# Performance work log

Measured on AMD Instinct MI355X. Metric: run time of the kernel, lower is better.

The kernel has to match this reference:

```python
import jax, jax.numpy as jnp
import numpy as np

B, S, D, H = 4, 2048, 512, 8

def setup_inputs() -> dict:
    key = jax.random.key(0)
    ks = jax.random.split(key, 6)
    query = jax.random.normal(ks[0], (B, S, D), dtype=jnp.float32)
    value = jax.random.normal(ks[1], (B, S, D), dtype=jnp.float32)
    # causal additive mask, broadcast over heads: [H, S, S]
    causal = jnp.where(jnp.tril(jnp.ones((S, S), dtype=bool)), 0.0, -1e9).astype(jnp.float32)
    mask = jnp.broadcast_to(causal[None, :, :], (H, S, S))
    sd = 1.0 / np.sqrt(D)
    Wq = jax.random.normal(ks[2], (D, D), dtype=jnp.float32) * sd
    Wkv = jax.random.normal(ks[3], (D, 2 * D), dtype=jnp.float32) * sd
    Wo = jax.random.normal(ks[4], (D, D), dtype=jnp.float32) * sd
    normalizer = jnp.asarray(1.0 / np.sqrt(D // H), dtype=jnp.float32)  # 1/sqrt(head_size)
    head_mults = jnp.ones((1, 1, H, 1), dtype=jnp.float32)
    return {"query": query, "value": value, "mask": mask, "Wq": Wq, "Wkv": Wkv,
            "Wo": Wo, "normalizer": normalizer, "head_mults": head_mults}

def reference(query, value, mask, Wq, Wkv, Wo, normalizer, head_mults):
    b, sq, d = query.shape
    h = head_mults.shape[2]
    q = (query @ Wq).reshape(b, sq, h, -1)                 # [b,q,h,hd]
    k, v = jnp.split(value @ Wkv, 2, axis=-1)
    sk = value.shape[1]
    k = k.reshape(b, sk, h, -1)
    v = v.reshape(b, sk, h, -1)
    score = jnp.einsum('bqhd,bkhd->bhqk', q, k) * normalizer
    score = score + mask[None, :, :, :]
    align = jax.nn.softmax(score, axis=-1)
    heads = jnp.einsum('bhqk,bkhd->bqhd', align, v)        # [b,q,h,hd]
    # cross-head normalization (over head axis, ddof=0 like tf.reduce_std)
    mean = jnp.mean(heads, axis=-2, keepdims=True)
    std = jnp.std(heads, axis=-2, keepdims=True)
    heads = (heads - mean) / (std + 0.01)
    heads = heads * head_mults
    out = heads.reshape(b, sq, d) @ Wo
    return out
```

## Files before the change

### kernel.cpp

```cpp
#include <hip/hip_runtime.h>


typedef float  f32x4  __attribute__((ext_vector_type(4)));
typedef __bf16 bf16x8 __attribute__((ext_vector_type(8)));
typedef short  s16x4  __attribute__((ext_vector_type(4)));
typedef unsigned short u16;

#define BS 2048
#define DD 512
#define NH 8

__device__ __forceinline__ u16 f2bf(float f) {
  union { float f; unsigned u; } v; v.f = f;
  unsigned r = v.u + 0x7fffu + ((v.u >> 16) & 1u);
  return (u16)(r >> 16);
}
__device__ __forceinline__ float bf2f(u16 b) {
  union { unsigned u; float f; } v; v.u = ((unsigned)b) << 16; return v.f;
}
__device__ __forceinline__ u16 cvt1(float f) {
  __bf16 h = (__bf16)f;
  return __builtin_bit_cast(u16, h);
}

__device__ __forceinline__ void gll16(const u16* g, u16* l) {
  __builtin_amdgcn_global_load_lds((const __attribute__((address_space(1))) void*)g,
                                   (__attribute__((address_space(3))) void*)l, 16, 0, 0);
}

__global__ __launch_bounds__(256) void prep(const float* __restrict__ query,
                                            const float* __restrict__ value,
                                            const float* __restrict__ Wq,
                                            const float* __restrict__ Wkv,
                                            const float* __restrict__ Wo,
                                            u16* __restrict__ Qf, u16* __restrict__ Vf,
                                            u16* __restrict__ WqT, u16* __restrict__ WkvT,
                                            u16* __restrict__ WoT) {
  __shared__ float Ts[64][65];
  const int t = threadIdx.x;
  int tb = blockIdx.x;
  if (tb < 2048) {
    const float* s = (tb < 1024) ? query : value;
    u16* d = (tb < 1024) ? Qf : Vf;
    long off = (long)(tb & 1023) * 4096 + (long)t * 16;
    const float* sp = s + off;
    float4 x0 = *(const float4*)sp;
    float4 x1 = *(const float4*)(sp + 4);
    float4 x2 = *(const float4*)(sp + 8);
    float4 x3 = *(const float4*)(sp + 12);
    bf16x8 o0, o1;
    o0[0] = (__bf16)x0.x; o0[1] = (__bf16)x0.y; o0[2] = (__bf16)x0.z; o0[3] = (__bf16)x0.w;
    o0[4] = (__bf16)x1.x; o0[5] = (__bf16)x1.y; o0[6] = (__bf16)x1.z; o0[7] = (__bf16)x1.w;
    o1[0] = (__bf16)x2.x; o1[1] = (__bf16)x2.y; o1[2] = (__bf16)x2.z; o1[3] = (__bf16)x2.w;
    o1[4] = (__bf16)x3.x; o1[5] = (__bf16)x3.y; o1[6] = (__bf16)x3.z; o1[7] = (__bf16)x3.w;
    u16* dp = d + off;
    *(bf16x8*)dp = o0;
    *(bf16x8*)(dp + 8) = o1;
    return;
  }
  tb -= 2048;
  const float* W; u16* Wt; int N, ntn;
  if (tb < 64)       { W = Wq;  Wt = WqT;  N = 512;  ntn = 8; }
  else if (tb < 192) { W = Wkv; Wt = WkvT; N = 1024; ntn = 16; tb -= 64; }
  else               { W = Wo;  Wt = WoT;  N = 512;  ntn = 8;  tb -= 192; }
  int tk = tb / ntn, tn = tb - tk * ntn;
  int r = t >> 2, c0 = (t & 3) * 16;
  const float* src = &W[(long)(tk * 64 + r) * N + tn * 64 + c0];
#pragma unroll
  for (int j = 0; j < 4; ++j) {
    float4 x = *(const float4*)(src + j * 4);
    Ts[r][c0 + j * 4 + 0] = x.x; Ts[r][c0 + j * 4 + 1] = x.y;
    Ts[r][c0 + j * 4 + 2] = x.z; Ts[r][c0 + j * 4 + 3] = x.w;
  }
  __syncthreads();
  u16* dst = &Wt[(long)(tn * 64 + r) * 512 + tk * 64 + c0];
#pragma unroll
  for (int m = 0; m < 4; ++m) {
    ushort4 o;
    o.x = f2bf(Ts[c0 + m * 4 + 0][r]); o.y = f2bf(Ts[c0 + m * 4 + 1][r]);
    o.z = f2bf(Ts[c0 + m * 4 + 2][r]); o.w = f2bf(Ts[c0 + m * 4 + 3][r]);
    *(ushort4*)(dst + m * 4) = o;
  }
}

__device__ __forceinline__ void gemm_core64(const u16* __restrict__ A,
                                            const u16* __restrict__ Bt,
                                            int m0, int n0, int K,
                                            u16* Al, u16* Bl, f32x4 acc[4][4]) {
  const int t = threadIdx.x;
  const int wv = t >> 6, ln = t & 63, qd = ln >> 4, l16 = ln & 15;
  const int rw = (wv & 1) * 64, cw = (wv >> 1) * 64;
  const int srB = wv * 16 + (ln >> 2), scB = (ln & 3) * 8;
  for (int k0 = 0; k0 < K; k0 += 64) {
    __syncthreads();
#pragma unroll
    for (int p = 0; p < 2; ++p)
#pragma unroll
      for (int c = 0; c < 2; ++c) {
        int r = c * 64 + srB;
        gll16(&A[(long)(m0 + r) * K + k0 + p * 32 + scB], &Al[p * 4096 + r * 32 + scB]);
      }
#pragma unroll
    for (int p = 0; p < 2; ++p)
#pragma unroll
      for (int c = 0; c < 2; ++c) {
        int r = c * 64 + srB;
        gll16(&Bt[(long)(n0 + r) * K + k0 + p * 32 + scB], &Bl[p * 4096 + r * 32 + scB]);
      }
    __syncthreads();
#pragma unroll
    for (int p = 0; p < 2; ++p) {
      bf16x8 af[4], bfr[4];
#pragma unroll
      for (int i = 0; i < 4; ++i)
        af[i] = *(const bf16x8*)&Al[p * 4096 + (rw + i * 16 + l16) * 32 + qd * 8];
#pragma unroll
      for (int j = 0; j < 4; ++j)
        bfr[j] = *(const bf16x8*)&Bl[p * 4096 + (cw + j * 16 + l16) * 32 + qd * 8];
#pragma unroll
      for (int i = 0; i < 4; ++i)
#pragma unroll
        for (int j = 0; j < 4; ++j)
          acc[i][j] = __builtin_amdgcn_mfma_f32_16x16x32_bf16(af[i], bfr[j], acc[i][j], 0, 0, 0);
    }
  }
}

__global__ __launch_bounds__(256) void qkv_gemm(const u16* __restrict__ Qf,
                                                const u16* __restrict__ Vf,
                                                const u16* __restrict__ WqT,
                                                const u16* __restrict__ WkvT,
                                                u16* __restrict__ Qb,
                                                u16* __restrict__ Kb,
                                                u16* __restrict__ Vt) {
  __shared__ __align__(16) u16 Al[2 * 128 * 32];
  __shared__ __align__(16) u16 Bl[2 * 128 * 32];
  const bool isQ = blockIdx.y < 4;
  const u16* A = isQ ? Qf : Vf;
  const u16* Bt = isQ ? WqT : WkvT;
  const int n0 = (isQ ? blockIdx.y : blockIdx.y - 4) * 128;
  const int m0 = blockIdx.x * 128;
  f32x4 acc[4][4] = {};
  gemm_core64(A, Bt, m0, n0, 512, Al, Bl, acc);
  const int t = threadIdx.x;
  const int wv = t >> 6, ln = t & 63, qd = ln >> 4, l16 = ln & 15;
  const int rw = (wv & 1) * 64, cw = (wv >> 1) * 64;
  if (isQ) {
#pragma unroll
    for (int i = 0; i < 4; ++i)
#pragma unroll
      for (int j = 0; j < 4; ++j) {
        int row = m0 + rw + i * 16 + qd * 4, col = n0 + cw + j * 16 + l16;
#pragma unroll
        for (int r = 0; r < 4; ++r)
          Qb[(long)(row + r) * 512 + col] = cvt1(acc[i][j][r]);
      }
  } else {
#pragma unroll
    for (int j = 0; j < 4; ++j) {
      int col = n0 + cw + j * 16 + l16;
      if (col < 512) {
#pragma unroll
        for (int i = 0; i < 4; ++i) {
          int row = m0 + rw + i * 16 + qd * 4;
#pragma unroll
          for (int r = 0; r < 4; ++r)
            Kb[(long)(row + r) * 512 + col] = cvt1(acc[i][j][r]);
        }
      } else {
        int c2 = col - 512, hh = c2 >> 6, dd = c2 & 63;
#pragma unroll
        for (int i = 0; i < 4; ++i) {
          int sg = m0 + rw + i * 16 + qd * 4;
          int bb = sg >> 11, ss = sg & 2047;
          ushort4 o;
          o.x = cvt1(acc[i][j][0]); o.y = cvt1(acc[i][j][1]);
          o.z = cvt1(acc[i][j][2]); o.w = cvt1(acc[i][j][3]);
          *(ushort4*)&Vt[((long)(bb * 8 + hh) * 64 + dd) * 2048 + ss] = o;
        }
      }
    }
  }
}

__global__ __launch_bounds__(256) void out_gemm(const u16* __restrict__ A,
                                                const u16* __restrict__ Bt,
                                                float* __restrict__ C) {
  __shared__ __align__(16) u16 Al[2 * 128 * 32];
  __shared__ __align__(16) u16 Bl[2 * 128 * 32];
  const int m0 = blockIdx.x * 128, n0 = blockIdx.y * 128;
  f32x4 acc[4][4] = {};
  gemm_core64(A, Bt, m0, n0, 512, Al, Bl, acc);
  const int t = threadIdx.x;
  const int wv = t >> 6, ln = t & 63, qd = ln >> 4, l16 = ln & 15;
  const int rw = (wv & 1) * 64, cw = (wv >> 1) * 64;
#pragma unroll
  for (int i = 0; i < 4; ++i)
#pragma unroll
    for (int j = 0; j < 4; ++j) {
      int row = m0 + rw + i * 16 + qd * 4, col = n0 + cw + j * 16 + l16;
#pragma unroll
      for (int r = 0; r < 4; ++r)
        C[(long)(row + r) * 512 + col] = acc[i][j][r];
    }
}

__device__ __forceinline__ void attn_phase(const u16* ks, const u16* vs,
                                           const bf16x8 bq[2], f32x4 o[4],
                                           float& l_i, float scale2, bool diag,
                                           int wv, int qd, int l16) {
  constexpr int ST = 72;
  f32x4 s[4] = {};
#pragma unroll
  for (int c = 0; c < 2; ++c)
#pragma unroll
    for (int nt = 0; nt < 4; ++nt) {
      bf16x8 ak = *(const bf16x8*)&ks[(nt * 16 + l16) * ST + c * 32 + qd * 8];
      s[nt] = __builtin_amdgcn_mfma_f32_16x16x32_bf16(ak, bq[c], s[nt], 0, 0, 0);
    }
  if (diag) {
    const int limi = wv * 16 + l16;
#pragma unroll
    for (int nt = 0; nt < 4; ++nt)
#pragma unroll
      for (int r = 0; r < 4; ++r) {
        float v = s[nt][r] * scale2;
        if (nt * 16 + qd * 4 + r > limi) v = -INFINITY;
        float p = exp2f(v);
        s[nt][r] = p;
        l_i += p;
      }
  } else {
#pragma unroll
    for (int nt = 0; nt < 4; ++nt)
#pragma unroll
      for (int r = 0; r < 4; ++r) {
        float p = exp2f(s[nt][r] * scale2);
        s[nt][r] = p;
        l_i += p;
      }
  }
#pragma unroll
  for (int cp = 0; cp < 2; ++cp) {
    bf16x8 pb;
#pragma unroll
    for (int j = 0; j < 4; ++j) {
      pb[j] = (__bf16)s[cp * 2][j];
      pb[4 + j] = (__bf16)s[cp * 2 + 1][j];
    }
#pragma unroll
    for (int n2 = 0; n2 < 4; ++n2) {
      bf16x8 av;
      s16x4* ah = (s16x4*)&av;
      const u16* vp = &vs[(n2 * 16 + l16) * ST + cp * 32 + qd * 4];
      ah[0] = *(const s16x4*)vp;
      ah[1] = *(const s16x4*)(vp + 16);
      o[n2] = __builtin_amdgcn_mfma_f32_16x16x32_bf16(av, pb, o[n2], 0, 0, 0);
    }
  }
}

__global__ __launch_bounds__(256, 2) void attn(const u16* __restrict__ Qb,
                                               const u16* __restrict__ Kb,
                                               const u16* __restrict__ Vt,
                                               u16* __restrict__ heads,
                                               const float* __restrict__ normp) {
  constexpr int ST = 72;
  __shared__ __align__(16) u16 Ks[2][64 * ST];
  __shared__ __align__(16) u16 Vts[2][64 * ST];
  const float scale2 = normp[0] * 1.44269504f;
  const int t = threadIdx.x;
  const int wv = t >> 6, ln = t & 63, qd = ln >> 4, l16 = ln & 15;
  const int sr = t >> 2, scg = (t & 3) * 16;
  const int h = blockIdx.y, b = blockIdx.z;
  const int bs0 = b * BS;
  const u16* vtb = Vt + ((long)(b * 8 + h) * 64) * 2048;
  const int qtS = blockIdx.x, qtL = 31 - qtS;

  bf16x8 bqS[2], bqL[2];
#pragma unroll
  for (int c = 0; c < 2; ++c) {
    bqS[c] = *(const bf16x8*)&Qb[(long)(bs0 + qtS * 64 + wv * 16 + l16) * 512 + h * 64 + c * 32 + qd * 8];
    bqL[c] = *(const bf16x8*)&Qb[(long)(bs0 + qtL * 64 + wv * 16 + l16) * 512 + h * 64 + c * 32 + qd * 8];
  }

  bf16x8 kr0, kr1, vr0, vr1;
#define FETCH(KB) do { \
    const u16* kp_ = &Kb[(long)(bs0 + (KB) * 64 + sr) * 512 + h * 64 + scg]; \
    kr0 = *(const bf16x8*)kp_; kr1 = *(const bf16x8*)(kp_ + 8); \
    const u16* vp_ = &vtb[(long)sr * 2048 + (KB) * 64 + scg]; \
    vr0 = *(const bf16x8*)vp_; vr1 = *(const bf16x8*)(vp_ + 8); } while (0)
  FETCH(0);
  float lS = 0.f, lL = 0.f;
  f32x4 oS[4] = {}, oL[4] = {};

  for (int kb = 0; kb <= qtL; ++kb) {
    const int buf = kb & 1;
    *(bf16x8*)&Ks[buf][sr * ST + scg] = kr0;
    *(bf16x8*)&Ks[buf][sr * ST + scg + 8] = kr1;
    *(bf16x8*)&Vts[buf][sr * ST + scg] = vr0;
    *(bf16x8*)&Vts[buf][sr * ST + scg + 8] = vr1;
    __syncthreads();
    if (kb < qtL) FETCH(kb + 1);

    attn_phase(Ks[buf], Vts[buf], bqL, oL, lL, scale2, kb == qtL, wv, qd, l16);
    if (kb <= qtS)
      attn_phase(Ks[buf], Vts[buf], bqS, oS, lS, scale2, kb == qtS, wv, qd, l16);
  }
#undef FETCH

  lL += __shfl_xor(lL, 16); lL += __shfl_xor(lL, 32);
  lS += __shfl_xor(lS, 16); lS += __shfl_xor(lS, 32);
  float invL = 1.f / lL, invS = 1.f / lS;
  __syncthreads();
#pragma unroll
  for (int n2 = 0; n2 < 4; ++n2)
#pragma unroll
    for (int r = 0; r < 4; ++r) {
      Ks[0][(wv * 16 + l16) * ST + n2 * 16 + qd * 4 + r] = cvt1(oL[n2][r] * invL);
      Vts[0][(wv * 16 + l16) * ST + n2 * 16 + qd * 4 + r] = cvt1(oS[n2][r] * invS);
    }
  __syncthreads();
  {
    u16* dstL = &heads[(long)(bs0 + qtL * 64 + sr) * 512 + h * 64 + scg];
    *(bf16x8*)dstL = *(const bf16x8*)&Ks[0][sr * ST + scg];
    *(bf16x8*)(dstL + 8) = *(const bf16x8*)&Ks[0][sr * ST + scg + 8];
    u16* dstS = &heads[(long)(bs0 + qtS * 64 + sr) * 512 + h * 64 + scg];
    *(bf16x8*)dstS = *(const bf16x8*)&Vts[0][sr * ST + scg];
    *(bf16x8*)(dstS + 8) = *(const bf16x8*)&Vts[0][sr * ST + scg + 8];
  }
}

__global__ __launch_bounds__(256) void headnorm(const u16* __restrict__ heads,
                                                const float* __restrict__ hm,
                                                u16* __restrict__ outn) {
  int i = blockIdx.x * 256 + threadIdx.x;
  int d8 = (i & 7) * 8;
  long bs = i >> 3;
  const u16* p = heads + bs * DD + d8;
  float x[NH][8];
  float mean[8] = {0.f, 0.f, 0.f, 0.f, 0.f, 0.f, 0.f, 0.f};
#pragma unroll
  for (int h = 0; h < NH; ++h) {
    bf16x8 v = *(const bf16x8*)(p + h * 64);
#pragma unroll
    for (int j = 0; j < 8; ++j) { x[h][j] = (float)v[j]; mean[j] += x[h][j]; }
  }
#pragma unroll
  for (int j = 0; j < 8; ++j) mean[j] *= 0.125f;
  float var[8] = {0.f, 0.f, 0.f, 0.f, 0.f, 0.f, 0.f, 0.f};
#pragma unroll
  for (int h = 0; h < NH; ++h)
#pragma unroll
    for (int j = 0; j < 8; ++j) { float dd = x[h][j] - mean[j]; var[j] += dd * dd; }
  float inv[8];
#pragma unroll
  for (int j = 0; j < 8; ++j) inv[j] = 1.f / (sqrtf(var[j] * 0.125f) + 0.01f);
  u16* q = outn + bs * DD + d8;
#pragma unroll
  for (int h = 0; h < NH; ++h) {
    float m = hm[h];
    bf16x8 o;
#pragma unroll
    for (int j = 0; j < 8; ++j) o[j] = (__bf16)((x[h][j] - mean[j]) * inv[j] * m);
    *(bf16x8*)(q + h * 64) = o;
  }
}

extern "C" void kernel_launch(void* const* d_in, const int* in_sizes, int n_in,
                              void* d_out, int out_size, void* d_ws, size_t ws_size,
                              hipStream_t stream) {
  const float* query = (const float*)d_in[0];
  const float* value = (const float*)d_in[1];
  const float* Wq    = (const float*)d_in[3];
  const float* Wkv   = (const float*)d_in[4];
  const float* Wo    = (const float*)d_in[5];
  const float* normp = (const float*)d_in[6];
  const float* hmult = (const float*)d_in[7];

  char* ws = (char*)d_ws;
  const size_t MB = 1 << 20;
  u16*   WqT   = (u16*)(ws);
  u16*   WkvT  = (u16*)(ws + 524288);
  u16*   WoT   = (u16*)(ws + 1 * MB + 524288);
  u16*   Qb    = (u16*)(ws + 2 * MB);
  u16*   Kb    = (u16*)(ws + 10 * MB);
  u16*   Vt    = (u16*)(ws + 18 * MB);
  u16*   heads = (u16*)(ws + 26 * MB);
  u16*   hN    = (u16*)(ws + 34 * MB);
  u16*   Qf    = (u16*)(ws + 42 * MB);
  u16*   Vf    = (u16*)(ws + 50 * MB);

  prep<<<2304, 256, 0, stream>>>(query, value, Wq, Wkv, Wo, Qf, Vf, WqT, WkvT, WoT);
  qkv_gemm<<<dim3(64, 12), 256, 0, stream>>>(Qf, Vf, WqT, WkvT, Qb, Kb, Vt);
  attn<<<dim3(16, NH, 4), 256, 0, stream>>>(Qb, Kb, Vt, heads, normp);
  headnorm<<<(4 * BS * 64) / 512, 256, 0, stream>>>(heads, hmult, hN);
  out_gemm<<<dim3(64, 4), 256, 0, stream>>>(hN, WoT, (float*)d_out);
}
```

Measured before the change: 286.2 us.

## Split paired causal query tiles into one tile per block, raise occupancy

Each attention block used to process a short and a long query tile together to balance causal work, sharing K/V loads between them. Now each block handles a single 64-row query tile, the grid doubles to 32 tiles, and launch bounds request 4 blocks per CU. This gives more parallelism and lower register pressure, at the cost of losing K/V reuse across the paired tiles and leaving per-block work unbalanced, so the long tiles may dominate the tail.

Measured after the change: 307.4 us. +7.4%, slower.

```diff
diff --git a/kernel.cpp b/kernel.cpp
--- a/kernel.cpp
+++ b/kernel.cpp
@@ -260,7 +260,7 @@
   }
 }
 
-__global__ __launch_bounds__(256, 2) void attn(const u16* __restrict__ Qb,
+__global__ __launch_bounds__(256, 4) void attn(const u16* __restrict__ Qb,
                                                const u16* __restrict__ Kb,
                                                const u16* __restrict__ Vt,
                                                u16* __restrict__ heads,
@@ -275,14 +275,12 @@
   const int h = blockIdx.y, b = blockIdx.z;
   const int bs0 = b * BS;
   const u16* vtb = Vt + ((long)(b * 8 + h) * 64) * 2048;
-  const int qtS = blockIdx.x, qtL = 31 - qtS;
-
-  bf16x8 bqS[2], bqL[2];
-#pragma unroll
-  for (int c = 0; c < 2; ++c) {
-    bqS[c] = *(const bf16x8*)&Qb[(long)(bs0 + qtS * 64 + wv * 16 + l16) * 512 + h * 64 + c * 32 + qd * 8];
-    bqL[c] = *(const bf16x8*)&Qb[(long)(bs0 + qtL * 64 + wv * 16 + l16) * 512 + h * 64 + c * 32 + qd * 8];
-  }
+  const int qt = blockIdx.x;
+
+  bf16x8 bq[2];
+#pragma unroll
+  for (int c = 0; c < 2; ++c)
+    bq[c] = *(const bf16x8*)&Qb[(long)(bs0 + qt * 64 + wv * 16 + l16) * 512 + h * 64 + c * 32 + qd * 8];
 
   bf16x8 kr0, kr1, vr0, vr1;
 #define FETCH(KB) do { \
@@ -291,43 +289,35 @@
     const u16* vp_ = &vtb[(long)sr * 2048 + (KB) * 64 + scg]; \
     vr0 = *(const bf16x8*)vp_; vr1 = *(const bf16x8*)(vp_ + 8); } while (0)
   FETCH(0);
-  float lS = 0.f, lL = 0.f;
-  f32x4 oS[4] = {}, oL[4] = {};
-
-  for (int kb = 0; kb <= qtL; ++kb) {
+  float l_i = 0.f;
+  f32x4 o[4] = {};
+
+  for (int kb = 0; kb <= qt; ++kb) {
     const int buf = kb & 1;
     *(bf16x8*)&Ks[buf][sr * ST + scg] = kr0;
     *(bf16x8*)&Ks[buf][sr * ST + scg + 8] = kr1;
     *(bf16x8*)&Vts[buf][sr * ST + scg] = vr0;
     *(bf16x8*)&Vts[buf][sr * ST + scg + 8] = vr1;
     __syncthreads();
-    if (kb < qtL) FETCH(kb + 1);
-
-    attn_phase(Ks[buf], Vts[buf], bqL, oL, lL, scale2, kb == qtL, wv, qd, l16);
-    if (kb <= qtS)
-      attn_phase(Ks[buf], Vts[buf], bqS, oS, lS, scale2, kb == qtS, wv, qd, l16);
+    if (kb < qt) FETCH(kb + 1);
+
+    attn_phase(Ks[buf], Vts[buf], bq, o, l_i, scale2, kb == qt, wv, qd, l16);
   }
 #undef FETCH
 
-  lL += __shfl_xor(lL, 16); lL += __shfl_xor(lL, 32);
-  lS += __shfl_xor(lS, 16); lS += __shfl_xor(lS, 32);
-  float invL = 1.f / lL, invS = 1.f / lS;
+  l_i += __shfl_xor(l_i, 16); l_i += __shfl_xor(l_i, 32);
+  float inv = 1.f / l_i;
   __syncthreads();
 #pragma unroll
   for (int n2 = 0; n2 < 4; ++n2)
 #pragma unroll
-    for (int r = 0; r < 4; ++r) {
-      Ks[0][(wv * 16 + l16) * ST + n2 * 16 + qd * 4 + r] = cvt1(oL[n2][r] * invL);
-      Vts[0][(wv * 16 + l16) * ST + n2 * 16 + qd * 4 + r] = cvt1(oS[n2][r] * invS);
-    }
+    for (int r = 0; r < 4; ++r)
+      Ks[0][(wv * 16 + l16) * ST + n2 * 16 + qd * 4 + r] = cvt1(o[n2][r] * inv);
   __syncthreads();
   {
-    u16* dstL = &heads[(long)(bs0 + qtL * 64 + sr) * 512 + h * 64 + scg];
-    *(bf16x8*)dstL = *(const bf16x8*)&Ks[0][sr * ST + scg];
-    *(bf16x8*)(dstL + 8) = *(const bf16x8*)&Ks[0][sr * ST + scg + 8];
-    u16* dstS = &heads[(long)(bs0 + qtS * 64 + sr) * 512 + h * 64 + scg];
-    *(bf16x8*)dstS = *(const bf16x8*)&Vts[0][sr * ST + scg];
-    *(bf16x8*)(dstS + 8) = *(const bf16x8*)&Vts[0][sr * ST + scg + 8];
+    u16* dst = &heads[(long)(bs0 + qt * 64 + sr) * 512 + h * 64 + scg];
+    *(bf16x8*)dst = *(const bf16x8*)&Ks[0][sr * ST + scg];
+    *(bf16x8*)(dst + 8) = *(const bf16x8*)&Ks[0][sr * ST + scg + 8];
   }
 }
 
@@ -393,7 +383,7 @@
 
   prep<<<2304, 256, 0, stream>>>(query, value, Wq, Wkv, Wo, Qf, Vf, WqT, WkvT, WoT);
   qkv_gemm<<<dim3(64, 12), 256, 0, stream>>>(Qf, Vf, WqT, WkvT, Qb, Kb, Vt);
-  attn<<<dim3(16, NH, 4), 256, 0, stream>>>(Qb, Kb, Vt, heads, normp);
+  attn<<<dim3(32, NH, 4), 256, 0, stream>>>(Qb, Kb, Vt, heads, normp);
   headnorm<<<(4 * BS * 64) / 512, 256, 0, stream>>>(heads, hmult, hN);
   out_gemm<<<dim3(64, 4), 256, 0, stream>>>(hN, WoT, (float*)d_out);
 }
```
